# Kernel tuning notes

Measured on AMD Instinct MI355X. Metric: run time of the kernel, lower is better.

Reference implementation:

```python
import jax, jax.numpy as jnp
import numpy as np

N, D, H = 2048, 1024, 16
DH = D // H
LN_EPS = 1e-5


def setup_inputs() -> dict:
    key = jax.random.key(0)
    ks = jax.random.split(key, 12)
    s = 1.0 / np.sqrt(D)
    return {
        "ht": jax.random.normal(ks[0], (N, D), jnp.float32),
        "attention_mask": jnp.ones((1, N), jnp.float32),
        "Wq": jax.random.normal(ks[1], (D, D), jnp.float32) * s,
        "bq": jnp.zeros((D,), jnp.float32),
        "Wk": jax.random.normal(ks[2], (D, D), jnp.float32) * s,
        "bk": jnp.zeros((D,), jnp.float32),
        "Wv": jax.random.normal(ks[3], (D, D), jnp.float32) * s,
        "bv": jnp.zeros((D,), jnp.float32),
        "Wd": jax.random.normal(ks[4], (D, D), jnp.float32) * s,
        "bd": jnp.zeros((D,), jnp.float32),
        "gamma": jnp.ones((D,), jnp.float32),
        "beta": jnp.zeros((D,), jnp.float32),
    }


def reference(ht, attention_mask, Wq, bq, Wk, bk, Wv, bv, Wd, bd, gamma, beta):
    # ht: [N, D] -> batch of 1: [1, N, D]
    x = ht[None]
    # QKV projections, split into heads: [1, N, H, DH]
    q = (x @ Wq.T + bq).reshape(1, N, H, DH)
    k = (x @ Wk.T + bk).reshape(1, N, H, DH)
    v = (x @ Wv.T + bv).reshape(1, N, H, DH)
    # attention scores [1, H, N, N]
    scores = jnp.einsum("bnhd,bmhd->bhnm", q, k) / jnp.sqrt(jnp.asarray(DH, x.dtype))
    # 2D mask -> [B, 1, 1, N], additive form (1 - m) * -10000
    ext_mask = (1.0 - attention_mask)[:, None, None, :] * -10000.0
    scores = scores + ext_mask
    probs = jax.nn.softmax(scores, axis=-1)
    # context [1, N, H, DH] -> [N, D]
    ctx = jnp.einsum("bhnm,bmhd->bnhd", probs, v).reshape(1, N, D)[0]
    # dense + tanh (dropout p=0 is identity) + residual
    sht = jnp.tanh(ctx @ Wd.T + bd) + ht
    # LayerNorm over last dim
    mu = jnp.mean(sht, axis=-1, keepdims=True)
    var = jnp.var(sht, axis=-1, keepdims=True)
    return (sht - mu) / jnp.sqrt(var + LN_EPS) * gamma + beta
```

## Files before the change

kernel.cpp:

```cpp
#include <hip/hip_runtime.h>
#include <hip/hip_bf16.h>
#include <math.h>

#define N_TOK 2048
#define DMODEL 1024
#define NHEAD 16
#define DHEAD 64
#define LN_EPS 1e-5f
#define LOG2E 1.44269504f

typedef __attribute__((ext_vector_type(8))) short short8;
typedef __attribute__((ext_vector_type(4))) float f32x4;
typedef __attribute__((ext_vector_type(16))) float f32x16;

__device__ inline unsigned short f2bf(float f) {
    union { float f; unsigned u; } v; v.f = f;
    unsigned r = v.u + 0x7FFF + ((v.u >> 16) & 1);
    return (unsigned short)(r >> 16);
}

__device__ inline float bf2f(unsigned short b) {
    union { unsigned u; float f; } v; v.u = ((unsigned)b) << 16;
    return v.f;
}
// ... 74 lines not shown
    int srow = l >> 3;
    int ssc = (((l & 7) ^ srow) << 3);

    f32x4 acc[4][2] = {};

    for (int k0 = 0; k0 < DMODEL; k0 += 64) {
        #pragma unroll
        for (int c = 0; c < 2; ++c) {
            int ci = (w << 1) | c;
            int r = (ci << 3) | srow;
            gld16(X + (size_t)(row0 + r) * DMODEL + k0 + ssc, As + ci * 512);
        }
        #pragma unroll
        for (int c = 0; c < 4; ++c) {
            int ci = (w << 2) | c;
            int r = (ci << 3) | srow;
            gld16(W + (size_t)(wcol0 + r) * DMODEL + k0 + ssc, Bs + ci * 512);
        }
        __syncthreads();
        #pragma unroll
        for (int kk = 0; kk < 64; kk += 32) {
            short8 af[4], bf[2];
            #pragma unroll
            for (int m = 0; m < 4; ++m)
                af[m] = *reinterpret_cast<const short8*>(
                    As + (m * 16 + lr) * 64 + ((((kk >> 3) + lk) ^ (lr & 7)) << 3));
            #pragma unroll
            for (int n = 0; n < 2; ++n)
                bf[n] = *reinterpret_cast<const short8*>(
                    Bs + (wc + n * 16 + lr) * 64 + ((((kk >> 3) + lk) ^ (lr & 7)) << 3));
            #pragma unroll
            for (int m = 0; m < 4; ++m)
                #pragma unroll
                for (int n = 0; n < 2; ++n)
                    acc[m][n] = __builtin_amdgcn_mfma_f32_16x16x32_bf16(af[m], bf[n], acc[m][n], 0, 0, 0);
        }
        __syncthreads();
    }

    if (mat == 2) {
        #pragma unroll
        for (int n = 0; n < 2; ++n) {
            int dl = wc + n * 16 + lr;
            float bia = bias[wcol0 + dl];
            #pragma unroll
            for (int m = 0; m < 4; ++m) {
                #pragma unroll
                for (int r = 0; r < 4; ++r) {
                    int nl = m * 16 + lk * 4 + r;
                    Bs[dl * 72 + nl] = f2bf(acc[m][n][r] + bia);
                }
            }
        }
        __syncthreads();
        #pragma unroll
        for (int it = 0; it < 4; ++it) {
            int slot = it * 256 + t;
            int dl = slot >> 3, nb = slot & 7;
            short8 v = *reinterpret_cast<const short8*>(Bs + dl * 72 + nb * 8);
            *reinterpret_cast<short8*>(VT + (size_t)(wcol0 + dl) * N_TOK + row0 + nb * 8) = v;
        }
    } else {
        unsigned short* O = (mat == 0) ? Q : K;
        #pragma unroll
        for (int n = 0; n < 2; ++n) {
            int ccol = wcol0 + wc + n * 16 + lr;
            float bia = bias[ccol];
            #pragma unroll
            for (int m = 0; m < 4; ++m) {
                #pragma unroll
                for (int r = 0; r < 4; ++r) {
                    int rowg = row0 + m * 16 + lk * 4 + r;
                    O[(size_t)rowg * DMODEL + ccol] = f2bf((acc[m][n][r] + bia) * osc);
                }
            }
        }
    }
}

__global__ __launch_bounds__(256) void attn32(
    const unsigned short* __restrict__ Q, const unsigned short* __restrict__ K,
    const unsigned short* __restrict__ VT, const float* __restrict__ madd,
    unsigned short* __restrict__ P0, unsigned short* __restrict__ P1,
    float* __restrict__ Mm, float* __restrict__ Ml)
{
    __shared__ __align__(16) unsigned short Kt[2][2][4096];
    __shared__ __align__(16) unsigned short Vt[2][2][4096];
    __shared__ __align__(16) float Mt[2][128];

    int p = blockIdx.x;
    int work = (p & 7) * 64 + (p >> 3);
    int h = (work >> 4) & 15;
    int hb = h * DHEAD;
    int z = work >> 8;
    int kbase = z << 10;
    int t = threadIdx.x, w = t >> 6, l = t & 63;
    int lo5 = l & 31, hi = l >> 5;
    int qw = (work & 15) * 128 + w * 32;

    short8 qf[4];
    #pragma unroll
    for (int ds = 0; ds < 4; ++ds)
        qf[ds] = *reinterpret_cast<const short8*>(
            Q + (size_t)(qw + lo5) * DMODEL + hb + ds * 16 + hi * 8);

    short8 ones8;
    #pragma unroll
    for (int j = 0; j < 8; ++j) ones8[j] = (short)0x3F80;

    f32x16 ctx0 = {}, ctx1 = {}, ctxS = {};
    float mrow = -1e30f;

#define STAGE(kt_, buf_) do {                                                   \
        int k0s = kbase + (kt_) * 128;                                          \
        _Pragma("unroll")                                                       \
        for (int sub = 0; sub < 2; ++sub) {                                     \
            _Pragma("unroll")                                                   \
            for (int c = 0; c < 2; ++c) {                                       \
                int ci = (w << 1) | c;                                          \
                int rr = (ci << 3) | (l >> 3);                                  \
                int sc = (((l & 7) ^ (rr & 7)) << 3);                           \
                gld16(K + (size_t)(k0s + sub * 64 + rr) * DMODEL + hb + sc,     \
                      &Kt[buf_][sub][ci * 512]);                                \
                gld16(VT + (size_t)(hb + rr) * N_TOK + k0s + sub * 64 + sc,     \
                      &Vt[buf_][sub][ci * 512]);                                \
            }                                                                   \
        }                                                                       \
        if (t < 32) gld16((const unsigned short*)(madd + k0s + l * 4),          \
                          (unsigned short*)&Mt[buf_][0]);                       \
    } while (0)

    STAGE(0, 0);
    __syncthreads();

    int cb = 0;
    for (int kt = 0; kt < 8; ++kt) {
        if (kt + 1 < 8) STAGE(kt + 1, cb ^ 1);

        #pragma unroll
        for (int sub = 0; sub < 2; ++sub) {
            const unsigned short* Kc = &Kt[cb][sub][0];
            const unsigned short* Vc = &Vt[cb][sub][0];
            const float* Mc = &Mt[cb][sub * 64];

            f32x16 s0, s1;
            #pragma unroll
            for (int rg = 0; rg < 4; ++rg) {
                f32x4 a = *reinterpret_cast<const f32x4*>(Mc + 8 * rg + 4 * hi);
                f32x4 b = *reinterpret_cast<const f32x4*>(Mc + 32 + 8 * rg + 4 * hi);
                #pragma unroll
                for (int j = 0; j < 4; ++j) { s0[4 * rg + j] = a[j]; s1[4 * rg + j] = b[j]; }
            }

            __builtin_amdgcn_s_setprio(1);
            #pragma unroll
            for (int ds = 0; ds < 4; ++ds) {
                short8 a0 = *reinterpret_cast<const short8*>(
                    Kc + (size_t)lo5 * 64 + (((2 * ds + hi) ^ (l & 7)) << 3));
                s0 = __builtin_amdgcn_mfma_f32_32x32x16_bf16(a0, qf[ds], s0, 0, 0, 0);
            }
            #pragma unroll
            for (int ds = 0; ds < 4; ++ds) {
                short8 a1 = *reinterpret_cast<const short8*>(
                    Kc + (size_t)(32 + lo5) * 64 + (((2 * ds + hi) ^ (l & 7)) << 3));
                s1 = __builtin_amdgcn_mfma_f32_32x32x16_bf16(a1, qf[ds], s1, 0, 0, 0);
            }
            __builtin_amdgcn_s_setprio(0);

            float u0 = mx3(s0[0], s0[1], s0[2]);
            float u1 = mx3(s0[3], s0[4], s0[5]);
            float u2 = mx3(s0[6], s0[7], s0[8]);
            float u3 = mx3(s0[9], s0[10], s0[11]);
            float u4 = mx3(s0[12], s0[13], s0[14]);
            float u5 = mx3(s0[15], s1[0], s1[1]);
            float u6 = mx3(s1[2], s1[3], s1[4]);
            float u7 = mx3(s1[5], s1[6], s1[7]);
            float u8 = mx3(s1[8], s1[9], s1[10]);
            float u9 = mx3(s1[11], s1[12], s1[13]);
            float ua = fmaxf(s1[14], s1[15]);
            float v0_ = mx3(u0, u1, u2);
            float v1_ = mx3(u3, u4, u5);
            float v2_ = mx3(u6, u7, u8);
            float tm = mx3(v0_, v1_, mx3(v2_, u9, ua));
            tm = fmaxf(tm, __shfl_xor(tm, 32));

            if (__any(tm > mrow + 8.0f)) {
                float mnew = fmaxf(mrow, tm);
                float sc = __builtin_amdgcn_exp2f(mrow - mnew);
                mrow = mnew;
                #pragma unroll
                for (int reg = 0; reg < 16; ++reg) {
                    float scr = __shfl(sc, (reg & 3) + 8 * (reg >> 2) + 4 * hi);
                    ctx0[reg] *= scr; ctx1[reg] *= scr; ctxS[reg] *= scr;
                }
            }

            unsigned u[2][4][2];
            #pragma unroll
            for (int g = 0; g < 4; ++g) {
                float p0 = __builtin_amdgcn_exp2f(s0[4 * g + 0] - mrow);
                float p1 = __builtin_amdgcn_exp2f(s0[4 * g + 1] - mrow);
                float p2 = __builtin_amdgcn_exp2f(s0[4 * g + 2] - mrow);
                float p3 = __builtin_amdgcn_exp2f(s0[4 * g + 3] - mrow);
                u[0][g][0] = cvtpk_bf16(p0, p1);
                u[0][g][1] = cvtpk_bf16(p2, p3);
                float q0_ = __builtin_amdgcn_exp2f(s1[4 * g + 0] - mrow);
                float q1_ = __builtin_amdgcn_exp2f(s1[4 * g + 1] - mrow);
                float q2_ = __builtin_amdgcn_exp2f(s1[4 * g + 2] - mrow);
                float q3_ = __builtin_amdgcn_exp2f(s1[4 * g + 3] - mrow);
                u[1][g][0] = cvtpk_bf16(q0_, q1_);
                u[1][g][1] = cvtpk_bf16(q2_, q3_);
            }

            short8 pa[4];
            #pragma unroll
            for (int nb = 0; nb < 2; ++nb) {
                #pragma unroll
                for (int ks = 0; ks < 2; ++ks) {
                    auto r0 = __builtin_amdgcn_permlane32_swap(u[nb][2 * ks][0], u[nb][2 * ks + 1][0], false, false);
                    auto r1 = __builtin_amdgcn_permlane32_swap(u[nb][2 * ks][1], u[nb][2 * ks + 1][1], false, false);
                    union { unsigned uu[4]; short8 v; } pu;
                    pu.uu[0] = r0[0]; pu.uu[1] = r1[0]; pu.uu[2] = r0[1]; pu.uu[3] = r1[1];
                    pa[nb * 2 + ks] = pu.v;
                }
            }

            __builtin_amdgcn_s_setprio(1);
            #pragma unroll
            for (int ks = 0; ks < 4; ++ks) {
                short8 v0 = *reinterpret_cast<const short8*>(
                    Vc + (size_t)lo5 * 64 + (((2 * ks + hi) ^ (l & 7)) << 3));
                ctx0 = __builtin_amdgcn_mfma_f32_32x32x16_bf16(pa[ks], v0, ctx0, 0, 0, 0);
                short8 v1 = *reinterpret_cast<const short8*>(
                    Vc + (size_t)(32 + lo5) * 64 + (((2 * ks + hi) ^ (l & 7)) << 3));
                ctx1 = __builtin_amdgcn_mfma_f32_32x32x16_bf16(pa[ks], v1, ctx1, 0, 0, 0);
                ctxS = __builtin_amdgcn_mfma_f32_32x32x16_bf16(pa[ks], ones8, ctxS, 0, 0, 0);
            }
            __builtin_amdgcn_s_setprio(0);
        }

        __syncthreads();
        cb ^= 1;
    }
#undef STAGE

    unsigned short* P = z ? P1 : P0;
    #pragma unroll
    for (int reg = 0; reg < 16; ++reg) {
        float inv = 1.0f / ctxS[reg];
        int row = qw + (reg & 3) + 8 * (reg >> 2) + 4 * hi;
        P[(size_t)row * DMODEL + hb + lo5]      = f2bf(ctx0[reg] * inv);
        P[(size_t)row * DMODEL + hb + 32 + lo5] = f2bf(ctx1[reg] * inv);
    }
    int mlb = z * (NHEAD * N_TOK) + h * N_TOK + qw;
    if (l < 32) Mm[mlb + l] = mrow;
    #pragma unroll
    for (int reg = 0; reg < 16; ++reg) {
        int q = (reg & 3) + 8 * (reg >> 2) + 4 * hi;
        if (lo5 == reg) Ml[mlb + q] = ctxS[reg];
    }
}

__global__ __launch_bounds__(256) void attn_combine(
    const unsigned short* __restrict__ P0, const unsigned short* __restrict__ P1,
    const float* __restrict__ Mm, const float* __restrict__ Ml,
    unsigned short* __restrict__ Ctx)
{
    int tok = blockIdx.x;
    int t = threadIdx.x;
    int d = t * 4;
    int h = t >> 4;
    int i0 = h * N_TOK + tok;
    int i1 = NHEAD * N_TOK + i0;
    float m0 = Mm[i0], m1 = Mm[i1];
    float l0 = Ml[i0], l1 = Ml[i1];
    float m = fmaxf(m0, m1);
    float w0 = l0 * __builtin_amdgcn_exp2f(m0 - m);
    float w1 = l1 * __builtin_amdgcn_exp2f(m1 - m);
    float inv = 1.0f / (w0 + w1);
    w0 *= inv; w1 *= inv;
    ushort4 c0 = *reinterpret_cast<const ushort4*>(P0 + (size_t)tok * DMODEL + d);
    ushort4 c1 = *reinterpret_cast<const ushort4*>(P1 + (size_t)tok * DMODEL + d);
    ushort4 o;
    o.x = f2bf(bf2f(c0.x) * w0 + bf2f(c1.x) * w1);
    o.y = f2bf(bf2f(c0.y) * w0 + bf2f(c1.y) * w1);
    o.z = f2bf(bf2f(c0.z) * w0 + bf2f(c1.z) * w1);
    o.w = f2bf(bf2f(c0.w) * w0 + bf2f(c1.w) * w1);
    *reinterpret_cast<ushort4*>(Ctx + (size_t)tok * DMODEL + d) = o;
}

__global__ __launch_bounds__(256) void gemm_dense(
    const unsigned short* __restrict__ X, const unsigned short* __restrict__ W,
    const float* __restrict__ bias, const float* __restrict__ ht,
    float* __restrict__ Sht)
{
    __shared__ __align__(16) unsigned short As[64 * 64];
    __shared__ __align__(16) unsigned short Bs[64 * 64];
    int p = blockIdx.x;
    int work = (p & 7) * 64 + (p >> 3);
    int row0 = (work % 32) * 64;
    int col0 = (work / 32) * 64;

    int t = threadIdx.x, w = t >> 6, l = t & 63;
    int lr = l & 15, lk = l >> 4;
    int wc = w * 16;
    int srow = l >> 3;
    int ssc = (((l & 7) ^ srow) << 3);

    f32x4 acc[4] = {};

    for (int k0 = 0; k0 < DMODEL; k0 += 64) {
        #pragma unroll
        for (int c = 0; c < 2; ++c) {
            int ci = (w << 1) | c;
            int r = (ci << 3) | srow;
            gld16(X + (size_t)(row0 + r) * DMODEL + k0 + ssc, As + ci * 512);
            gld16(W + (size_t)(col0 + r) * DMODEL + k0 + ssc, Bs + ci * 512);
        }
        __syncthreads();
        #pragma unroll
        for (int kk = 0; kk < 64; kk += 32) {
            short8 af[4], bf0;
            #pragma unroll
            for (int m = 0; m < 4; ++m)
                af[m] = *reinterpret_cast<const short8*>(
                    As + (m * 16 + lr) * 64 + ((((kk >> 3) + lk) ^ (lr & 7)) << 3));
            bf0 = *reinterpret_cast<const short8*>(
                Bs + (wc + lr) * 64 + ((((kk >> 3) + lk) ^ (lr & 7)) << 3));
            #pragma unroll
            for (int m = 0; m < 4; ++m)
                acc[m] = __builtin_amdgcn_mfma_f32_16x16x32_bf16(af[m], bf0, acc[m], 0, 0, 0);
        }
        __syncthreads();
    }

    int col = col0 + wc + lr;
    float bia = bias[col];
    #pragma unroll
    for (int m = 0; m < 4; ++m) {
        #pragma unroll
        for (int r = 0; r < 4; ++r) {
            int rowg = row0 + m * 16 + lk * 4 + r;
            float x2 = 2.0f * (acc[m][r] + bia);
            float th = 1.0f - 2.0f / (1.0f + __expf(x2));
            Sht[(size_t)rowg * DMODEL + col] = th + ht[(size_t)rowg * DMODEL + col];
        }
    }
}

__global__ __launch_bounds__(256) void layernorm(
    const float* __restrict__ S, const float* __restrict__ gamma,
    const float* __restrict__ beta, float* __restrict__ out)
{
    int row = blockIdx.x;
    int t = threadIdx.x;
    const float* x = S + (size_t)row * DMODEL;
    float4 v = *reinterpret_cast<const float4*>(x + t * 4);
    float sum = v.x + v.y + v.z + v.w;
    float sq = v.x * v.x + v.y * v.y + v.z * v.z + v.w * v.w;
    #pragma unroll
    for (int d = 1; d < 64; d <<= 1) { sum += __shfl_xor(sum, d); sq += __shfl_xor(sq, d); }
    __shared__ float ssum[4], ssq[4];
    int w = t >> 6, l = t & 63;
    if (l == 0) { ssum[w] = sum; ssq[w] = sq; }
    __syncthreads();
    sum = ssum[0] + ssum[1] + ssum[2] + ssum[3];
    sq = ssq[0] + ssq[1] + ssq[2] + ssq[3];
    float mu = sum / DMODEL;
    float var = sq / DMODEL - mu * mu;
    float inv = rsqrtf(var + LN_EPS);
    float4 g = *reinterpret_cast<const float4*>(gamma + t * 4);
    float4 b = *reinterpret_cast<const float4*>(beta + t * 4);
    float4 o;
    o.x = (v.x - mu) * inv * g.x + b.x;
    o.y = (v.y - mu) * inv * g.y + b.y;
    o.z = (v.z - mu) * inv * g.z + b.z;
    o.w = (v.w - mu) * inv * g.w + b.w;
    *reinterpret_cast<float4*>(out + (size_t)row * DMODEL + t * 4) = o;
}

extern "C" void kernel_launch(void* const* d_in, const int* in_sizes, int n_in,
                              void* d_out, int out_size, void* d_ws, size_t ws_size,
                              hipStream_t stream) {
    const float* ht   = (const float*)d_in[0];
    const float* mask = (const float*)d_in[1];
    const float* Wq   = (const float*)d_in[2];
    const float* bq   = (const float*)d_in[3];
    const float* Wk   = (const float*)d_in[4];
    const float* bk   = (const float*)d_in[5];
    const float* Wv   = (const float*)d_in[6];
    const float* bv   = (const float*)d_in[7];
    const float* Wd   = (const float*)d_in[8];
    const float* bd   = (const float*)d_in[9];
    const float* gamma= (const float*)d_in[10];
    const float* beta = (const float*)d_in[11];
    float* out = (float*)d_out;

    char* ws = (char*)d_ws;
    const size_t MB = 1024 * 1024;
    unsigned short* Xb  = (unsigned short*)(ws + 0 * MB);
    unsigned short* Wqb = (unsigned short*)(ws + 4 * MB);
    unsigned short* Wkb = (unsigned short*)(ws + 6 * MB);
    unsigned short* Wvb = (unsigned short*)(ws + 8 * MB);
    unsigned short* Wdb = (unsigned short*)(ws + 10 * MB);
    unsigned short* Qb  = (unsigned short*)(ws + 12 * MB);
    unsigned short* Kb  = (unsigned short*)(ws + 16 * MB);
    unsigned short* Vb  = (unsigned short*)(ws + 20 * MB);
    unsigned short* VTb = (unsigned short*)(ws + 24 * MB);
    unsigned short* Ctxb= (unsigned short*)(ws + 28 * MB);
    float* maddb        = (float*)(ws + 32 * MB);
    unsigned short* Pctx0 = Xb;
    unsigned short* Pctx1 = Vb;
    float* Mm           = (float*)(ws + 4 * MB);
    float* Ml           = (float*)(ws + 4 * MB + 256 * 1024);
    float* Sht          = (float*)(ws + 12 * MB);

    cvt_all<<<6146, 256, 0, stream>>>(ht, Wq, Wk, Wv, Wd, mask,
                                      Xb, Wqb, Wkb, Wvb, Wdb, maddb);

    gemm_qkv<<<768, 256, 0, stream>>>(Xb, Wqb, Wkb, Wvb, bq, bk, bv, Qb, Kb, VTb);

    attn32<<<512, 256, 0, stream>>>(Qb, Kb, VTb, maddb, Pctx0, Pctx1, Mm, Ml);

    attn_combine<<<N_TOK, 256, 0, stream>>>(Pctx0, Pctx1, Mm, Ml, Ctxb);

    gemm_dense<<<512, 256, 0, stream>>>(Ctxb, Wdb, bd, ht, Sht);

    layernorm<<<N_TOK, 256, 0, stream>>>(Sht, gamma, beta, out);
}
```

Measured before the change: 84.25 us.

## Split attention KV range four ways instead of two for more blocks

Raises the flash-decoding style KV split from 2 to 4 chunks of 512 keys, doubling the attention grid to 1024 blocks, with each block handling 64-key tiles and preloading its whole mask slice once. The combine kernel now merges four partial contexts using per-split max and sum. The goal is better CU occupancy and latency hiding on the attention pass. In exchange it adds more partial-output traffic and combine work, shrinks the per-iteration tile, and reshuffles workspace aliasing (Wqb, VTb and others reused as scratch).

```diff
diff --git a/kernel.cpp b/kernel.cpp
--- a/kernel.cpp
+++ b/kernel.cpp
@@ -180,18 +180,19 @@
     const unsigned short* __restrict__ Q, const unsigned short* __restrict__ K,
     const unsigned short* __restrict__ VT, const float* __restrict__ madd,
     unsigned short* __restrict__ P0, unsigned short* __restrict__ P1,
+    unsigned short* __restrict__ P2, unsigned short* __restrict__ P3,
     float* __restrict__ Mm, float* __restrict__ Ml)
 {
-    __shared__ __align__(16) unsigned short Kt[2][2][4096];
-    __shared__ __align__(16) unsigned short Vt[2][2][4096];
-    __shared__ __align__(16) float Mt[2][128];
+    __shared__ __align__(16) unsigned short Kt[2][4096];
+    __shared__ __align__(16) unsigned short Vt[2][4096];
+    __shared__ __align__(16) float Mt[512];
 
     int p = blockIdx.x;
-    int work = (p & 7) * 64 + (p >> 3);
+    int work = (p & 7) * 128 + (p >> 3);
     int h = (work >> 4) & 15;
     int hb = h * DHEAD;
     int z = work >> 8;
-    int kbase = z << 10;
+    int kbase = z << 9;
     int t = threadIdx.x, w = t >> 6, l = t & 63;
     int lo5 = l & 31, hi = l >> 5;
     int qw = (work & 15) * 128 + w * 32;
@@ -209,23 +210,21 @@
     f32x16 ctx0 = {}, ctx1 = {}, ctxS = {};
     float mrow = -1e30f;
 
+    if (t < 128) {
+        gld16((const unsigned short*)(madd + kbase + t * 4),
+              (unsigned short*)&Mt[(t >> 6) * 256]);
+    }
+
 #define STAGE(kt_, buf_) do {                                                   \
-        int k0s = kbase + (kt_) * 128;                                          \
+        int k0s = kbase + (kt_) * 64;                                           \
         _Pragma("unroll")                                                       \
-        for (int sub = 0; sub < 2; ++sub) {                                     \
-            _Pragma("unroll")                                                   \
-            for (int c = 0; c < 2; ++c) {                                       \
-                int ci = (w << 1) | c;                                          \
-                int rr = (ci << 3) | (l >> 3);                                  \
-                int sc = (((l & 7) ^ (rr & 7)) << 3);                           \
-                gld16(K + (size_t)(k0s + sub * 64 + rr) * DMODEL + hb + sc,     \
-                      &Kt[buf_][sub][ci * 512]);                                \
-                gld16(VT + (size_t)(hb + rr) * N_TOK + k0s + sub * 64 + sc,     \
-                      &Vt[buf_][sub][ci * 512]);                                \
-            }                                                                   \
+        for (int c = 0; c < 2; ++c) {                                           \
+            int ci = (w << 1) | c;                                              \
+            int rr = (ci << 3) | (l >> 3);                                      \
+            int sc = (((l & 7) ^ (rr & 7)) << 3);                               \
+            gld16(K + (size_t)(k0s + rr) * DMODEL + hb + sc, &Kt[buf_][ci * 512]); \
+            gld16(VT + (size_t)(hb + rr) * N_TOK + k0s + sc, &Vt[buf_][ci * 512]); \
         }                                                                       \
-        if (t < 32) gld16((const unsigned short*)(madd + k0s + l * 4),          \
-                          (unsigned short*)&Mt[buf_][0]);                       \
     } while (0)
 
     STAGE(0, 0);
@@ -235,114 +234,111 @@
     for (int kt = 0; kt < 8; ++kt) {
         if (kt + 1 < 8) STAGE(kt + 1, cb ^ 1);
 
-        #pragma unroll
-        for (int sub = 0; sub < 2; ++sub) {
-            const unsigned short* Kc = &Kt[cb][sub][0];
-            const unsigned short* Vc = &Vt[cb][sub][0];
-            const float* Mc = &Mt[cb][sub * 64];
-
-            f32x16 s0, s1;
-            #pragma unroll
-            for (int rg = 0; rg < 4; ++rg) {
-                f32x4 a = *reinterpret_cast<const f32x4*>(Mc + 8 * rg + 4 * hi);
-                f32x4 b = *reinterpret_cast<const f32x4*>(Mc + 32 + 8 * rg + 4 * hi);
-                #pragma unroll
-                for (int j = 0; j < 4; ++j) { s0[4 * rg + j] = a[j]; s1[4 * rg + j] = b[j]; }
+        const unsigned short* Kc = &Kt[cb][0];
+        const unsigned short* Vc = &Vt[cb][0];
+        const float* Mc = &Mt[kt * 64];
+
+        f32x16 s0, s1;
+        #pragma unroll
+        for (int rg = 0; rg < 4; ++rg) {
+            f32x4 a = *reinterpret_cast<const f32x4*>(Mc + 8 * rg + 4 * hi);
+            f32x4 b = *reinterpret_cast<const f32x4*>(Mc + 32 + 8 * rg + 4 * hi);
+            #pragma unroll
+            for (int j = 0; j < 4; ++j) { s0[4 * rg + j] = a[j]; s1[4 * rg + j] = b[j]; }
+        }
+
+        __builtin_amdgcn_s_setprio(1);
+        #pragma unroll
+        for (int ds = 0; ds < 4; ++ds) {
+            short8 a0 = *reinterpret_cast<const short8*>(
+                Kc + (size_t)lo5 * 64 + (((2 * ds + hi) ^ (l & 7)) << 3));
+            s0 = __builtin_amdgcn_mfma_f32_32x32x16_bf16(a0, qf[ds], s0, 0, 0, 0);
+        }
+        #pragma unroll
+        for (int ds = 0; ds < 4; ++ds) {
+            short8 a1 = *reinterpret_cast<const short8*>(
+                Kc + (size_t)(32 + lo5) * 64 + (((2 * ds + hi) ^ (l & 7)) << 3));
+            s1 = __builtin_amdgcn_mfma_f32_32x32x16_bf16(a1, qf[ds], s1, 0, 0, 0);
+        }
+        __builtin_amdgcn_s_setprio(0);
+
+        float u0 = mx3(s0[0], s0[1], s0[2]);
+        float u1 = mx3(s0[3], s0[4], s0[5]);
+        float u2 = mx3(s0[6], s0[7], s0[8]);
+        float u3 = mx3(s0[9], s0[10], s0[11]);
+        float u4 = mx3(s0[12], s0[13], s0[14]);
+        float u5 = mx3(s0[15], s1[0], s1[1]);
+        float u6 = mx3(s1[2], s1[3], s1[4]);
+        float u7 = mx3(s1[5], s1[6], s1[7]);
+        float u8 = mx3(s1[8], s1[9], s1[10]);
+        float u9 = mx3(s1[11], s1[12], s1[13]);
+        float ua = fmaxf(s1[14], s1[15]);
+        float v0_ = mx3(u0, u1, u2);
+        float v1_ = mx3(u3, u4, u5);
+        float v2_ = mx3(u6, u7, u8);
+        float tm = mx3(v0_, v1_, mx3(v2_, u9, ua));
+        tm = fmaxf(tm, __shfl_xor(tm, 32));
+
+        if (__any(tm > mrow + 8.0f)) {
+            float mnew = fmaxf(mrow, tm);
+            float sc = __builtin_amdgcn_exp2f(mrow - mnew);
+            mrow = mnew;
+            #pragma unroll
+            for (int reg = 0; reg < 16; ++reg) {
+                float scr = __shfl(sc, (reg & 3) + 8 * (reg >> 2) + 4 * hi);
+                ctx0[reg] *= scr; ctx1[reg] *= scr; ctxS[reg] *= scr;
             }
-
-            __builtin_amdgcn_s_setprio(1);
-            #pragma unroll
-            for (int ds = 0; ds < 4; ++ds) {
-                short8 a0 = *reinterpret_cast<const short8*>(
-                    Kc + (size_t)lo5 * 64 + (((2 * ds + hi) ^ (l & 7)) << 3));
-                s0 = __builtin_amdgcn_mfma_f32_32x32x16_bf16(a0, qf[ds], s0, 0, 0, 0);
+        }
+
+        unsigned u[2][4][2];
+        #pragma unroll
+        for (int g = 0; g < 4; ++g) {
+            float p0 = __builtin_amdgcn_exp2f(s0[4 * g + 0] - mrow);
+            float p1 = __builtin_amdgcn_exp2f(s0[4 * g + 1] - mrow);
+            float p2 = __builtin_amdgcn_exp2f(s0[4 * g + 2] - mrow);
+            float p3 = __builtin_amdgcn_exp2f(s0[4 * g + 3] - mrow);
+            u[0][g][0] = cvtpk_bf16(p0, p1);
+            u[0][g][1] = cvtpk_bf16(p2, p3);
+            float q0_ = __builtin_amdgcn_exp2f(s1[4 * g + 0] - mrow);
+            float q1_ = __builtin_amdgcn_exp2f(s1[4 * g + 1] - mrow);
+            float q2_ = __builtin_amdgcn_exp2f(s1[4 * g + 2] - mrow);
+            float q3_ = __builtin_amdgcn_exp2f(s1[4 * g + 3] - mrow);
+            u[1][g][0] = cvtpk_bf16(q0_, q1_);
+            u[1][g][1] = cvtpk_bf16(q2_, q3_);
+        }
+
+        short8 pa[4];
+        #pragma unroll
+        for (int nb = 0; nb < 2; ++nb) {
+            #pragma unroll
+            for (int ks = 0; ks < 2; ++ks) {
+                auto r0 = __builtin_amdgcn_permlane32_swap(u[nb][2 * ks][0], u[nb][2 * ks + 1][0], false, false);
+                auto r1 = __builtin_amdgcn_permlane32_swap(u[nb][2 * ks][1], u[nb][2 * ks + 1][1], false, false);
+                union { unsigned uu[4]; short8 v; } pu;
+                pu.uu[0] = r0[0]; pu.uu[1] = r1[0]; pu.uu[2] = r0[1]; pu.uu[3] = r1[1];
+                pa[nb * 2 + ks] = pu.v;
             }
-            #pragma unroll
-            for (int ds = 0; ds < 4; ++ds) {
-                short8 a1 = *reinterpret_cast<const short8*>(
-                    Kc + (size_t)(32 + lo5) * 64 + (((2 * ds + hi) ^ (l & 7)) << 3));
-                s1 = __builtin_amdgcn_mfma_f32_32x32x16_bf16(a1, qf[ds], s1, 0, 0, 0);
-            }
-            __builtin_amdgcn_s_setprio(0);
-
-            float u0 = mx3(s0[0], s0[1], s0[2]);
-            float u1 = mx3(s0[3], s0[4], s0[5]);
-            float u2 = mx3(s0[6], s0[7], s0[8]);
-            float u3 = mx3(s0[9], s0[10], s0[11]);
-            float u4 = mx3(s0[12], s0[13], s0[14]);
-            float u5 = mx3(s0[15], s1[0], s1[1]);
-            float u6 = mx3(s1[2], s1[3], s1[4]);
-            float u7 = mx3(s1[5], s1[6], s1[7]);
-            float u8 = mx3(s1[8], s1[9], s1[10]);
-            float u9 = mx3(s1[11], s1[12], s1[13]);
-            float ua = fmaxf(s1[14], s1[15]);
-            float v0_ = mx3(u0, u1, u2);
-            float v1_ = mx3(u3, u4, u5);
-            float v2_ = mx3(u6, u7, u8);
-            float tm = mx3(v0_, v1_, mx3(v2_, u9, ua));
-            tm = fmaxf(tm, __shfl_xor(tm, 32));
-
-            if (__any(tm > mrow + 8.0f)) {
-                float mnew = fmaxf(mrow, tm);
-                float sc = __builtin_amdgcn_exp2f(mrow - mnew);
-                mrow = mnew;
-                #pragma unroll
-                for (int reg = 0; reg < 16; ++reg) {
-                    float scr = __shfl(sc, (reg & 3) + 8 * (reg >> 2) + 4 * hi);
-                    ctx0[reg] *= scr; ctx1[reg] *= scr; ctxS[reg] *= scr;
-                }
-            }
-
-            unsigned u[2][4][2];
-            #pragma unroll
-            for (int g = 0; g < 4; ++g) {
-                float p0 = __builtin_amdgcn_exp2f(s0[4 * g + 0] - mrow);
-                float p1 = __builtin_amdgcn_exp2f(s0[4 * g + 1] - mrow);
-                float p2 = __builtin_amdgcn_exp2f(s0[4 * g + 2] - mrow);
-                float p3 = __builtin_amdgcn_exp2f(s0[4 * g + 3] - mrow);
-                u[0][g][0] = cvtpk_bf16(p0, p1);
-                u[0][g][1] = cvtpk_bf16(p2, p3);
-                float q0_ = __builtin_amdgcn_exp2f(s1[4 * g + 0] - mrow);
-                float q1_ = __builtin_amdgcn_exp2f(s1[4 * g + 1] - mrow);
-                float q2_ = __builtin_amdgcn_exp2f(s1[4 * g + 2] - mrow);
-                float q3_ = __builtin_amdgcn_exp2f(s1[4 * g + 3] - mrow);
-                u[1][g][0] = cvtpk_bf16(q0_, q1_);
-                u[1][g][1] = cvtpk_bf16(q2_, q3_);
-            }
-
-            short8 pa[4];
-            #pragma unroll
-            for (int nb = 0; nb < 2; ++nb) {
-                #pragma unroll
-                for (int ks = 0; ks < 2; ++ks) {
-                    auto r0 = __builtin_amdgcn_permlane32_swap(u[nb][2 * ks][0], u[nb][2 * ks + 1][0], false, false);
-                    auto r1 = __builtin_amdgcn_permlane32_swap(u[nb][2 * ks][1], u[nb][2 * ks + 1][1], false, false);
-                    union { unsigned uu[4]; short8 v; } pu;
-                    pu.uu[0] = r0[0]; pu.uu[1] = r1[0]; pu.uu[2] = r0[1]; pu.uu[3] = r1[1];
-                    pa[nb * 2 + ks] = pu.v;
-                }
-            }
-
-            __builtin_amdgcn_s_setprio(1);
-            #pragma unroll
-            for (int ks = 0; ks < 4; ++ks) {
-                short8 v0 = *reinterpret_cast<const short8*>(
-                    Vc + (size_t)lo5 * 64 + (((2 * ks + hi) ^ (l & 7)) << 3));
-                ctx0 = __builtin_amdgcn_mfma_f32_32x32x16_bf16(pa[ks], v0, ctx0, 0, 0, 0);
-                short8 v1 = *reinterpret_cast<const short8*>(
-                    Vc + (size_t)(32 + lo5) * 64 + (((2 * ks + hi) ^ (l & 7)) << 3));
-                ctx1 = __builtin_amdgcn_mfma_f32_32x32x16_bf16(pa[ks], v1, ctx1, 0, 0, 0);
-                ctxS = __builtin_amdgcn_mfma_f32_32x32x16_bf16(pa[ks], ones8, ctxS, 0, 0, 0);
-            }
-            __builtin_amdgcn_s_setprio(0);
-        }
+        }
+
+        __builtin_amdgcn_s_setprio(1);
+        #pragma unroll
+        for (int ks = 0; ks < 4; ++ks) {
+            short8 v0 = *reinterpret_cast<const short8*>(
+                Vc + (size_t)lo5 * 64 + (((2 * ks + hi) ^ (l & 7)) << 3));
+            ctx0 = __builtin_amdgcn_mfma_f32_32x32x16_bf16(pa[ks], v0, ctx0, 0, 0, 0);
+            short8 v1 = *reinterpret_cast<const short8*>(
+                Vc + (size_t)(32 + lo5) * 64 + (((2 * ks + hi) ^ (l & 7)) << 3));
+            ctx1 = __builtin_amdgcn_mfma_f32_32x32x16_bf16(pa[ks], v1, ctx1, 0, 0, 0);
+            ctxS = __builtin_amdgcn_mfma_f32_32x32x16_bf16(pa[ks], ones8, ctxS, 0, 0, 0);
+        }
+        __builtin_amdgcn_s_setprio(0);
 
         __syncthreads();
         cb ^= 1;
     }
 #undef STAGE
 
-    unsigned short* P = z ? P1 : P0;
+    unsigned short* P = (z == 0) ? P0 : (z == 1) ? P1 : (z == 2) ? P2 : P3;
     #pragma unroll
     for (int reg = 0; reg < 16; ++reg) {
         float inv = 1.0f / ctxS[reg];
@@ -361,6 +357,7 @@
 
 __global__ __launch_bounds__(256) void attn_combine(
     const unsigned short* __restrict__ P0, const unsigned short* __restrict__ P1,
+    const unsigned short* __restrict__ P2, const unsigned short* __restrict__ P3,
     const float* __restrict__ Mm, const float* __restrict__ Ml,
     unsigned short* __restrict__ Ctx)
 {
@@ -369,21 +366,25 @@
     int d = t * 4;
     int h = t >> 4;
     int i0 = h * N_TOK + tok;
-    int i1 = NHEAD * N_TOK + i0;
-    float m0 = Mm[i0], m1 = Mm[i1];
-    float l0 = Ml[i0], l1 = Ml[i1];
-    float m = fmaxf(m0, m1);
+    const int S = NHEAD * N_TOK;
+    float m0 = Mm[i0], m1 = Mm[i0 + S], m2 = Mm[i0 + 2 * S], m3 = Mm[i0 + 3 * S];
+    float l0 = Ml[i0], l1 = Ml[i0 + S], l2 = Ml[i0 + 2 * S], l3 = Ml[i0 + 3 * S];
+    float m = fmaxf(fmaxf(m0, m1), fmaxf(m2, m3));
     float w0 = l0 * __builtin_amdgcn_exp2f(m0 - m);
     float w1 = l1 * __builtin_amdgcn_exp2f(m1 - m);
-    float inv = 1.0f / (w0 + w1);
-    w0 *= inv; w1 *= inv;
+    float w2 = l2 * __builtin_amdgcn_exp2f(m2 - m);
+    float w3 = l3 * __builtin_amdgcn_exp2f(m3 - m);
+    float inv = 1.0f / (w0 + w1 + w2 + w3);
+    w0 *= inv; w1 *= inv; w2 *= inv; w3 *= inv;
     ushort4 c0 = *reinterpret_cast<const ushort4*>(P0 + (size_t)tok * DMODEL + d);
     ushort4 c1 = *reinterpret_cast<const ushort4*>(P1 + (size_t)tok * DMODEL + d);
+    ushort4 c2 = *reinterpret_cast<const ushort4*>(P2 + (size_t)tok * DMODEL + d);
+    ushort4 c3 = *reinterpret_cast<const ushort4*>(P3 + (size_t)tok * DMODEL + d);
     ushort4 o;
-    o.x = f2bf(bf2f(c0.x) * w0 + bf2f(c1.x) * w1);
-    o.y = f2bf(bf2f(c0.y) * w0 + bf2f(c1.y) * w1);
-    o.z = f2bf(bf2f(c0.z) * w0 + bf2f(c1.z) * w1);
-    o.w = f2bf(bf2f(c0.w) * w0 + bf2f(c1.w) * w1);
+    o.x = f2bf(bf2f(c0.x) * w0 + bf2f(c1.x) * w1 + bf2f(c2.x) * w2 + bf2f(c3.x) * w3);
+    o.y = f2bf(bf2f(c0.y) * w0 + bf2f(c1.y) * w1 + bf2f(c2.y) * w2 + bf2f(c3.y) * w3);
+    o.z = f2bf(bf2f(c0.z) * w0 + bf2f(c1.z) * w1 + bf2f(c2.z) * w2 + bf2f(c3.z) * w3);
+    o.w = f2bf(bf2f(c0.w) * w0 + bf2f(c1.w) * w1 + bf2f(c2.w) * w2 + bf2f(c3.w) * w3);
     *reinterpret_cast<ushort4*>(Ctx + (size_t)tok * DMODEL + d) = o;
 }
 
@@ -505,12 +506,14 @@
     unsigned short* Kb  = (unsigned short*)(ws + 16 * MB);
     unsigned short* Vb  = (unsigned short*)(ws + 20 * MB);
     unsigned short* VTb = (unsigned short*)(ws + 24 * MB);
-    unsigned short* Ctxb= (unsigned short*)(ws + 28 * MB);
     float* maddb        = (float*)(ws + 32 * MB);
     unsigned short* Pctx0 = Xb;
     unsigned short* Pctx1 = Vb;
-    float* Mm           = (float*)(ws + 4 * MB);
-    float* Ml           = (float*)(ws + 4 * MB + 256 * 1024);
+    unsigned short* Pctx2 = Wqb;
+    unsigned short* Pctx3 = (unsigned short*)(ws + 28 * MB);
+    float* Mm           = (float*)(ws + 8 * MB);
+    float* Ml           = (float*)(ws + 8 * MB + 512 * 1024);
+    unsigned short* Ctxb= VTb;
     float* Sht          = (float*)(ws + 12 * MB);
 
     cvt_all<<<6146, 256, 0, stream>>>(ht, Wq, Wk, Wv, Wd, mask,
@@ -518,9 +521,10 @@
 
     gemm_qkv<<<768, 256, 0, stream>>>(Xb, Wqb, Wkb, Wvb, bq, bk, bv, Qb, Kb, VTb);
 
-    attn32<<<512, 256, 0, stream>>>(Qb, Kb, VTb, maddb, Pctx0, Pctx1, Mm, Ml);
-
-    attn_combine<<<N_TOK, 256, 0, stream>>>(Pctx0, Pctx1, Mm, Ml, Ctxb);
+    attn32<<<1024, 256, 0, stream>>>(Qb, Kb, VTb, maddb,
+                                     Pctx0, Pctx1, Pctx2, Pctx3, Mm, Ml);
+
+    attn_combine<<<N_TOK, 256, 0, stream>>>(Pctx0, Pctx1, Pctx2, Pctx3, Mm, Ml, Ctxb);
 
     gemm_dense<<<512, 256, 0, stream>>>(Ctxb, Wdb, bd, ht, Sht);
 
```

Result: slower. 90.13 us (+7.0%).

## Triple-buffer K/V tiles with 64-key stages and explicit vmcnt waits in attention

Applied to the files above, without the earlier changes.

Restructures the attention kernel's K/V staging from double-buffered 128-key tiles to a three-slot ring of 64-key tiles, prefetching two stages ahead. The full 1024-entry mask slice is loaded once up front instead of per stage. __syncthreads is replaced with raw s_barrier plus s_waitcnt vmcnt counts, so a new load can be issued while earlier ones are still outstanding. This aims to hide global-load latency better at similar LDS use, but it adds more barriers per key and depends on the hand-counted vmcnt values being correct.

```diff
diff --git a/kernel.cpp b/kernel.cpp
--- a/kernel.cpp
+++ b/kernel.cpp
@@ -182,9 +182,9 @@
     unsigned short* __restrict__ P0, unsigned short* __restrict__ P1,
     float* __restrict__ Mm, float* __restrict__ Ml)
 {
-    __shared__ __align__(16) unsigned short Kt[2][2][4096];
-    __shared__ __align__(16) unsigned short Vt[2][2][4096];
-    __shared__ __align__(16) float Mt[2][128];
+    __shared__ __align__(16) unsigned short Kt[3][4096];
+    __shared__ __align__(16) unsigned short Vt[3][4096];
+    __shared__ __align__(16) float Mt[1024];
 
     int p = blockIdx.x;
     int work = (p & 7) * 64 + (p >> 3);
@@ -210,135 +210,140 @@
     float mrow = -1e30f;
 
 #define STAGE(kt_, buf_) do {                                                   \
-        int k0s = kbase + (kt_) * 128;                                          \
+        int k0s = kbase + (kt_) * 64;                                           \
         _Pragma("unroll")                                                       \
-        for (int sub = 0; sub < 2; ++sub) {                                     \
-            _Pragma("unroll")                                                   \
-            for (int c = 0; c < 2; ++c) {                                       \
-                int ci = (w << 1) | c;                                          \
-                int rr = (ci << 3) | (l >> 3);                                  \
-                int sc = (((l & 7) ^ (rr & 7)) << 3);                           \
-                gld16(K + (size_t)(k0s + sub * 64 + rr) * DMODEL + hb + sc,     \
-                      &Kt[buf_][sub][ci * 512]);                                \
-                gld16(VT + (size_t)(hb + rr) * N_TOK + k0s + sub * 64 + sc,     \
-                      &Vt[buf_][sub][ci * 512]);                                \
-            }                                                                   \
+        for (int c = 0; c < 2; ++c) {                                           \
+            int ci = (w << 1) | c;                                              \
+            int rr = (ci << 3) | (l >> 3);                                      \
+            int sc = (((l & 7) ^ (rr & 7)) << 3);                               \
+            gld16(K + (size_t)(k0s + rr) * DMODEL + hb + sc, &Kt[buf_][ci * 512]); \
+            gld16(VT + (size_t)(hb + rr) * N_TOK + k0s + sc, &Vt[buf_][ci * 512]); \
         }                                                                       \
-        if (t < 32) gld16((const unsigned short*)(madd + k0s + l * 4),          \
-                          (unsigned short*)&Mt[buf_][0]);                       \
     } while (0)
 
+    gld16((const unsigned short*)(madd + kbase + t * 4), (unsigned short*)&Mt[w * 256]);
     STAGE(0, 0);
-    __syncthreads();
+    STAGE(1, 1);
+    __builtin_amdgcn_sched_barrier(0);
+    asm volatile("s_waitcnt vmcnt(4)");
+    __builtin_amdgcn_s_barrier();
+    __builtin_amdgcn_sched_barrier(0);
 
     int cb = 0;
-    for (int kt = 0; kt < 8; ++kt) {
-        if (kt + 1 < 8) STAGE(kt + 1, cb ^ 1);
-
-        #pragma unroll
-        for (int sub = 0; sub < 2; ++sub) {
-            const unsigned short* Kc = &Kt[cb][sub][0];
-            const unsigned short* Vc = &Vt[cb][sub][0];
-            const float* Mc = &Mt[cb][sub * 64];
-
-            f32x16 s0, s1;
-            #pragma unroll
-            for (int rg = 0; rg < 4; ++rg) {
-                f32x4 a = *reinterpret_cast<const f32x4*>(Mc + 8 * rg + 4 * hi);
-                f32x4 b = *reinterpret_cast<const f32x4*>(Mc + 32 + 8 * rg + 4 * hi);
-                #pragma unroll
-                for (int j = 0; j < 4; ++j) { s0[4 * rg + j] = a[j]; s1[4 * rg + j] = b[j]; }
+    for (int kt = 0; kt < 16; ++kt) {
+        const unsigned short* Kc = &Kt[cb][0];
+        const unsigned short* Vc = &Vt[cb][0];
+        const float* Mc = &Mt[kt * 64];
+
+        f32x16 s0, s1;
+        #pragma unroll
+        for (int rg = 0; rg < 4; ++rg) {
+            f32x4 a = *reinterpret_cast<const f32x4*>(Mc + 8 * rg + 4 * hi);
+            f32x4 b = *reinterpret_cast<const f32x4*>(Mc + 32 + 8 * rg + 4 * hi);
+            #pragma unroll
+            for (int j = 0; j < 4; ++j) { s0[4 * rg + j] = a[j]; s1[4 * rg + j] = b[j]; }
+        }
+
+        __builtin_amdgcn_s_setprio(1);
+        #pragma unroll
+        for (int ds = 0; ds < 4; ++ds) {
+            short8 a0 = *reinterpret_cast<const short8*>(
+                Kc + (size_t)lo5 * 64 + (((2 * ds + hi) ^ (l & 7)) << 3));
+            s0 = __builtin_amdgcn_mfma_f32_32x32x16_bf16(a0, qf[ds], s0, 0, 0, 0);
+        }
+        #pragma unroll
+        for (int ds = 0; ds < 4; ++ds) {
+            short8 a1 = *reinterpret_cast<const short8*>(
+                Kc + (size_t)(32 + lo5) * 64 + (((2 * ds + hi) ^ (l & 7)) << 3));
+            s1 = __builtin_amdgcn_mfma_f32_32x32x16_bf16(a1, qf[ds], s1, 0, 0, 0);
+        }
+        __builtin_amdgcn_s_setprio(0);
+
+        float u0 = mx3(s0[0], s0[1], s0[2]);
+        float u1 = mx3(s0[3], s0[4], s0[5]);
+        float u2 = mx3(s0[6], s0[7], s0[8]);
+        float u3 = mx3(s0[9], s0[10], s0[11]);
+        float u4 = mx3(s0[12], s0[13], s0[14]);
+        float u5 = mx3(s0[15], s1[0], s1[1]);
+        float u6 = mx3(s1[2], s1[3], s1[4]);
+        float u7 = mx3(s1[5], s1[6], s1[7]);
+        float u8 = mx3(s1[8], s1[9], s1[10]);
+        float u9 = mx3(s1[11], s1[12], s1[13]);
+        float ua = fmaxf(s1[14], s1[15]);
+        float v0_ = mx3(u0, u1, u2);
+        float v1_ = mx3(u3, u4, u5);
+        float v2_ = mx3(u6, u7, u8);
+        float tm = mx3(v0_, v1_, mx3(v2_, u9, ua));
+        tm = fmaxf(tm, __shfl_xor(tm, 32));
+
+        if (__any(tm > mrow + 8.0f)) {
+            float mnew = fmaxf(mrow, tm);
+            float sc = __builtin_amdgcn_exp2f(mrow - mnew);
+            mrow = mnew;
+            #pragma unroll
+            for (int reg = 0; reg < 16; ++reg) {
+                float scr = __shfl(sc, (reg & 3) + 8 * (reg >> 2) + 4 * hi);
+                ctx0[reg] *= scr; ctx1[reg] *= scr; ctxS[reg] *= scr;
             }
-
-            __builtin_amdgcn_s_setprio(1);
-            #pragma unroll
-            for (int ds = 0; ds < 4; ++ds) {
-                short8 a0 = *reinterpret_cast<const short8*>(
-                    Kc + (size_t)lo5 * 64 + (((2 * ds + hi) ^ (l & 7)) << 3));
-                s0 = __builtin_amdgcn_mfma_f32_32x32x16_bf16(a0, qf[ds], s0, 0, 0, 0);
+        }
+
+        unsigned u[2][4][2];
+        #pragma unroll
+        for (int g = 0; g < 4; ++g) {
+            float p0 = __builtin_amdgcn_exp2f(s0[4 * g + 0] - mrow);
+            float p1 = __builtin_amdgcn_exp2f(s0[4 * g + 1] - mrow);
+            float p2 = __builtin_amdgcn_exp2f(s0[4 * g + 2] - mrow);
+            float p3 = __builtin_amdgcn_exp2f(s0[4 * g + 3] - mrow);
+            u[0][g][0] = cvtpk_bf16(p0, p1);
+            u[0][g][1] = cvtpk_bf16(p2, p3);
+            float q0_ = __builtin_amdgcn_exp2f(s1[4 * g + 0] - mrow);
+            float q1_ = __builtin_amdgcn_exp2f(s1[4 * g + 1] - mrow);
+            float q2_ = __builtin_amdgcn_exp2f(s1[4 * g + 2] - mrow);
+            float q3_ = __builtin_amdgcn_exp2f(s1[4 * g + 3] - mrow);
+            u[1][g][0] = cvtpk_bf16(q0_, q1_);
+            u[1][g][1] = cvtpk_bf16(q2_, q3_);
+        }
+
+        short8 pa[4];
+        #pragma unroll
+        for (int nb = 0; nb < 2; ++nb) {
+            #pragma unroll
+            for (int ks = 0; ks < 2; ++ks) {
+                auto r0 = __builtin_amdgcn_permlane32_swap(u[nb][2 * ks][0], u[nb][2 * ks + 1][0], false, false);
+                auto r1 = __builtin_amdgcn_permlane32_swap(u[nb][2 * ks][1], u[nb][2 * ks + 1][1], false, false);
+                union { unsigned uu[4]; short8 v; } pu;
+                pu.uu[0] = r0[0]; pu.uu[1] = r1[0]; pu.uu[2] = r0[1]; pu.uu[3] = r1[1];
+                pa[nb * 2 + ks] = pu.v;
             }
-            #pragma unroll
-            for (int ds = 0; ds < 4; ++ds) {
-                short8 a1 = *reinterpret_cast<const short8*>(
-                    Kc + (size_t)(32 + lo5) * 64 + (((2 * ds + hi) ^ (l & 7)) << 3));
-                s1 = __builtin_amdgcn_mfma_f32_32x32x16_bf16(a1, qf[ds], s1, 0, 0, 0);
-            }
-            __builtin_amdgcn_s_setprio(0);
-
-            float u0 = mx3(s0[0], s0[1], s0[2]);
-            float u1 = mx3(s0[3], s0[4], s0[5]);
-            float u2 = mx3(s0[6], s0[7], s0[8]);
-            float u3 = mx3(s0[9], s0[10], s0[11]);
-            float u4 = mx3(s0[12], s0[13], s0[14]);
-            float u5 = mx3(s0[15], s1[0], s1[1]);
-            float u6 = mx3(s1[2], s1[3], s1[4]);
-            float u7 = mx3(s1[5], s1[6], s1[7]);
-            float u8 = mx3(s1[8], s1[9], s1[10]);
-            float u9 = mx3(s1[11], s1[12], s1[13]);
-            float ua = fmaxf(s1[14], s1[15]);
-            float v0_ = mx3(u0, u1, u2);
-            float v1_ = mx3(u3, u4, u5);
-            float v2_ = mx3(u6, u7, u8);
-            float tm = mx3(v0_, v1_, mx3(v2_, u9, ua));
-            tm = fmaxf(tm, __shfl_xor(tm, 32));
-
-            if (__any(tm > mrow + 8.0f)) {
-                float mnew = fmaxf(mrow, tm);
-                float sc = __builtin_amdgcn_exp2f(mrow - mnew);
-                mrow = mnew;
-                #pragma unroll
-                for (int reg = 0; reg < 16; ++reg) {
-                    float scr = __shfl(sc, (reg & 3) + 8 * (reg >> 2) + 4 * hi);
-                    ctx0[reg] *= scr; ctx1[reg] *= scr; ctxS[reg] *= scr;
-                }
-            }
-
-            unsigned u[2][4][2];
-            #pragma unroll
-            for (int g = 0; g < 4; ++g) {
-                float p0 = __builtin_amdgcn_exp2f(s0[4 * g + 0] - mrow);
-                float p1 = __builtin_amdgcn_exp2f(s0[4 * g + 1] - mrow);
-                float p2 = __builtin_amdgcn_exp2f(s0[4 * g + 2] - mrow);
-                float p3 = __builtin_amdgcn_exp2f(s0[4 * g + 3] - mrow);
-                u[0][g][0] = cvtpk_bf16(p0, p1);
-                u[0][g][1] = cvtpk_bf16(p2, p3);
-                float q0_ = __builtin_amdgcn_exp2f(s1[4 * g + 0] - mrow);
-                float q1_ = __builtin_amdgcn_exp2f(s1[4 * g + 1] - mrow);
-                float q2_ = __builtin_amdgcn_exp2f(s1[4 * g + 2] - mrow);
-                float q3_ = __builtin_amdgcn_exp2f(s1[4 * g + 3] - mrow);
-                u[1][g][0] = cvtpk_bf16(q0_, q1_);
-                u[1][g][1] = cvtpk_bf16(q2_, q3_);
-            }
-
-            short8 pa[4];
-            #pragma unroll
-            for (int nb = 0; nb < 2; ++nb) {
-                #pragma unroll
-                for (int ks = 0; ks < 2; ++ks) {
-                    auto r0 = __builtin_amdgcn_permlane32_swap(u[nb][2 * ks][0], u[nb][2 * ks + 1][0], false, false);
-                    auto r1 = __builtin_amdgcn_permlane32_swap(u[nb][2 * ks][1], u[nb][2 * ks + 1][1], false, false);
-                    union { unsigned uu[4]; short8 v; } pu;
-                    pu.uu[0] = r0[0]; pu.uu[1] = r1[0]; pu.uu[2] = r0[1]; pu.uu[3] = r1[1];
-                    pa[nb * 2 + ks] = pu.v;
-                }
-            }
-
-            __builtin_amdgcn_s_setprio(1);
-            #pragma unroll
-            for (int ks = 0; ks < 4; ++ks) {
-                short8 v0 = *reinterpret_cast<const short8*>(
-                    Vc + (size_t)lo5 * 64 + (((2 * ks + hi) ^ (l & 7)) << 3));
-                ctx0 = __builtin_amdgcn_mfma_f32_32x32x16_bf16(pa[ks], v0, ctx0, 0, 0, 0);
-                short8 v1 = *reinterpret_cast<const short8*>(
-                    Vc + (size_t)(32 + lo5) * 64 + (((2 * ks + hi) ^ (l & 7)) << 3));
-                ctx1 = __builtin_amdgcn_mfma_f32_32x32x16_bf16(pa[ks], v1, ctx1, 0, 0, 0);
-                ctxS = __builtin_amdgcn_mfma_f32_32x32x16_bf16(pa[ks], ones8, ctxS, 0, 0, 0);
-            }
-            __builtin_amdgcn_s_setprio(0);
-        }
-
-        __syncthreads();
-        cb ^= 1;
+        }
+
+        __builtin_amdgcn_s_setprio(1);
+        #pragma unroll
+        for (int ks = 0; ks < 4; ++ks) {
+            short8 v0 = *reinterpret_cast<const short8*>(
+                Vc + (size_t)lo5 * 64 + (((2 * ks + hi) ^ (l & 7)) << 3));
+            ctx0 = __builtin_amdgcn_mfma_f32_32x32x16_bf16(pa[ks], v0, ctx0, 0, 0, 0);
+            short8 v1 = *reinterpret_cast<const short8*>(
+                Vc + (size_t)(32 + lo5) * 64 + (((2 * ks + hi) ^ (l & 7)) << 3));
+            ctx1 = __builtin_amdgcn_mfma_f32_32x32x16_bf16(pa[ks], v1, ctx1, 0, 0, 0);
+            ctxS = __builtin_amdgcn_mfma_f32_32x32x16_bf16(pa[ks], ones8, ctxS, 0, 0, 0);
+        }
+        __builtin_amdgcn_s_setprio(0);
+
+        __builtin_amdgcn_s_barrier();
+        __builtin_amdgcn_sched_barrier(0);
+        if (kt + 2 < 16) {
+            int sb = cb + 2; if (sb >= 3) sb -= 3;
+            STAGE(kt + 2, sb);
+        }
+        if (kt + 1 < 16) {
+            __builtin_amdgcn_sched_barrier(0);
+            if (kt + 2 < 16) asm volatile("s_waitcnt vmcnt(4)");
+            else             asm volatile("s_waitcnt vmcnt(0)");
+            __builtin_amdgcn_s_barrier();
+            __builtin_amdgcn_sched_barrier(0);
+        }
+        cb = (cb == 2) ? 0 : cb + 1;
     }
 #undef STAGE
 
```

Result: no change. 84.40 us (+0.2%).

## Fuse split-KV attention combine into dense GEMM A-tile staging with double buffering

Applied to the files above, without the earlier changes.

Removes the separate attn_combine kernel. The dense GEMM now loads both partial context tiles and their softmax max/sum statistics, merges them in registers, and writes the combined bf16 A tile into shared memory. The main loop is restructured with double-buffered LDS, so the next tile's loads overlap the current MFMA work. This saves one launch and one full round trip of the context tensor through memory. In exchange, each GEMM block now redoes the combine for every column tile and reads the partials more times, and it uses more registers and LDS.

```diff
diff --git a/kernel.cpp b/kernel.cpp
--- a/kernel.cpp
+++ b/kernel.cpp
@@ -359,41 +359,14 @@
     }
 }
 
-__global__ __launch_bounds__(256) void attn_combine(
+__global__ __launch_bounds__(256) void gemm_dense(
     const unsigned short* __restrict__ P0, const unsigned short* __restrict__ P1,
     const float* __restrict__ Mm, const float* __restrict__ Ml,
-    unsigned short* __restrict__ Ctx)
+    const unsigned short* __restrict__ W, const float* __restrict__ bias,
+    const float* __restrict__ ht, float* __restrict__ Sht)
 {
-    int tok = blockIdx.x;
-    int t = threadIdx.x;
-    int d = t * 4;
-    int h = t >> 4;
-    int i0 = h * N_TOK + tok;
-    int i1 = NHEAD * N_TOK + i0;
-    float m0 = Mm[i0], m1 = Mm[i1];
-    float l0 = Ml[i0], l1 = Ml[i1];
-    float m = fmaxf(m0, m1);
-    float w0 = l0 * __builtin_amdgcn_exp2f(m0 - m);
-    float w1 = l1 * __builtin_amdgcn_exp2f(m1 - m);
-    float inv = 1.0f / (w0 + w1);
-    w0 *= inv; w1 *= inv;
-    ushort4 c0 = *reinterpret_cast<const ushort4*>(P0 + (size_t)tok * DMODEL + d);
-    ushort4 c1 = *reinterpret_cast<const ushort4*>(P1 + (size_t)tok * DMODEL + d);
-    ushort4 o;
-    o.x = f2bf(bf2f(c0.x) * w0 + bf2f(c1.x) * w1);
-    o.y = f2bf(bf2f(c0.y) * w0 + bf2f(c1.y) * w1);
-    o.z = f2bf(bf2f(c0.z) * w0 + bf2f(c1.z) * w1);
-    o.w = f2bf(bf2f(c0.w) * w0 + bf2f(c1.w) * w1);
-    *reinterpret_cast<ushort4*>(Ctx + (size_t)tok * DMODEL + d) = o;
-}
-
-__global__ __launch_bounds__(256) void gemm_dense(
-    const unsigned short* __restrict__ X, const unsigned short* __restrict__ W,
-    const float* __restrict__ bias, const float* __restrict__ ht,
-    float* __restrict__ Sht)
-{
-    __shared__ __align__(16) unsigned short As[64 * 64];
-    __shared__ __align__(16) unsigned short Bs[64 * 64];
+    __shared__ __align__(16) unsigned short As[2][64 * 64];
+    __shared__ __align__(16) unsigned short Bs[2][64 * 64];
     int p = blockIdx.x;
     int work = (p & 7) * 64 + (p >> 3);
     int row0 = (work % 32) * 64;
@@ -405,32 +378,89 @@
     int srow = l >> 3;
     int ssc = (((l & 7) ^ srow) << 3);
 
+    int r_[2], c8_[2];
+    #pragma unroll
+    for (int it = 0; it < 2; ++it) { int slot = it * 256 + t; r_[it] = slot >> 3; c8_[it] = slot & 7; }
+
     f32x4 acc[4] = {};
 
-    for (int k0 = 0; k0 < DMODEL; k0 += 64) {
-        #pragma unroll
-        for (int c = 0; c < 2; ++c) {
-            int ci = (w << 1) | c;
-            int r = (ci << 3) | srow;
-            gld16(X + (size_t)(row0 + r) * DMODEL + k0 + ssc, As + ci * 512);
-            gld16(W + (size_t)(col0 + r) * DMODEL + k0 + ssc, Bs + ci * 512);
-        }
-        __syncthreads();
+    short8 a0[2], a1[2];
+    float pm0[2], pm1[2], pl0[2], pl1[2];
+
+#define LOADA(k0_) do {                                                          \
+        _Pragma("unroll")                                                        \
+        for (int it = 0; it < 2; ++it) {                                         \
+            int tok = row0 + r_[it];                                             \
+            int i0 = ((k0_) >> 6) * N_TOK + tok;                                 \
+            int i1 = NHEAD * N_TOK + i0;                                         \
+            a0[it] = *reinterpret_cast<const short8*>(P0 + (size_t)tok * DMODEL + (k0_) + c8_[it] * 8); \
+            a1[it] = *reinterpret_cast<const short8*>(P1 + (size_t)tok * DMODEL + (k0_) + c8_[it] * 8); \
+            pm0[it] = Mm[i0]; pm1[it] = Mm[i1];                                  \
+            pl0[it] = Ml[i0]; pl1[it] = Ml[i1];                                  \
+        }                                                                        \
+    } while (0)
+
+#define WRITEA(buf_) do {                                                        \
+        _Pragma("unroll")                                                        \
+        for (int it = 0; it < 2; ++it) {                                         \
+            float mm = fmaxf(pm0[it], pm1[it]);                                  \
+            float w0_ = pl0[it] * __builtin_amdgcn_exp2f(pm0[it] - mm);          \
+            float w1_ = pl1[it] * __builtin_amdgcn_exp2f(pm1[it] - mm);          \
+            float inv_ = 1.0f / (w0_ + w1_);                                     \
+            w0_ *= inv_; w1_ *= inv_;                                            \
+            union { unsigned uu[4]; short8 v; } pu;                              \
+            _Pragma("unroll")                                                    \
+            for (int j = 0; j < 4; ++j) {                                        \
+                float e0 = bf2f((unsigned short)a0[it][2 * j]) * w0_             \
+                         + bf2f((unsigned short)a1[it][2 * j]) * w1_;            \
+                float e1 = bf2f((unsigned short)a0[it][2 * j + 1]) * w0_         \
+                         + bf2f((unsigned short)a1[it][2 * j + 1]) * w1_;        \
+                pu.uu[j] = cvtpk_bf16(e0, e1);                                   \
+            }                                                                    \
+            *reinterpret_cast<short8*>(                                          \
+                &As[buf_][r_[it] * 64 + ((c8_[it] ^ (r_[it] & 7)) << 3)]) = pu.v;\
+        }                                                                        \
+    } while (0)
+
+#define STAGEB(k0_, buf_) do {                                                   \
+        _Pragma("unroll")                                                        \
+        for (int c = 0; c < 2; ++c) {                                            \
+            int ci = (w << 1) | c;                                               \
+            int rr = (ci << 3) | srow;                                           \
+            gld16(W + (size_t)(col0 + rr) * DMODEL + (k0_) + ssc, &Bs[buf_][ci * 512]); \
+        }                                                                        \
+    } while (0)
+
+    LOADA(0);
+    STAGEB(0, 0);
+    WRITEA(0);
+    __syncthreads();
+
+    for (int k0i = 0; k0i < 16; ++k0i) {
+        int buf = k0i & 1;
+        bool more = (k0i + 1) < 16;
+        if (more) { LOADA((k0i + 1) * 64); STAGEB((k0i + 1) * 64, buf ^ 1); }
+
         #pragma unroll
         for (int kk = 0; kk < 64; kk += 32) {
             short8 af[4], bf0;
             #pragma unroll
             for (int m = 0; m < 4; ++m)
                 af[m] = *reinterpret_cast<const short8*>(
-                    As + (m * 16 + lr) * 64 + ((((kk >> 3) + lk) ^ (lr & 7)) << 3));
+                    &As[buf][(m * 16 + lr) * 64 + ((((kk >> 3) + lk) ^ (lr & 7)) << 3)]);
             bf0 = *reinterpret_cast<const short8*>(
-                Bs + (wc + lr) * 64 + ((((kk >> 3) + lk) ^ (lr & 7)) << 3));
+                &Bs[buf][(wc + lr) * 64 + ((((kk >> 3) + lk) ^ (lr & 7)) << 3)]);
             #pragma unroll
             for (int m = 0; m < 4; ++m)
                 acc[m] = __builtin_amdgcn_mfma_f32_16x16x32_bf16(af[m], bf0, acc[m], 0, 0, 0);
         }
+
+        if (more) WRITEA(buf ^ 1);
         __syncthreads();
     }
+#undef LOADA
+#undef WRITEA
+#undef STAGEB
 
     int col = col0 + wc + lr;
     float bia = bias[col];
@@ -505,7 +535,6 @@
     unsigned short* Kb  = (unsigned short*)(ws + 16 * MB);
     unsigned short* Vb  = (unsigned short*)(ws + 20 * MB);
     unsigned short* VTb = (unsigned short*)(ws + 24 * MB);
-    unsigned short* Ctxb= (unsigned short*)(ws + 28 * MB);
     float* maddb        = (float*)(ws + 32 * MB);
     unsigned short* Pctx0 = Xb;
     unsigned short* Pctx1 = Vb;
@@ -520,9 +549,7 @@
 
     attn32<<<512, 256, 0, stream>>>(Qb, Kb, VTb, maddb, Pctx0, Pctx1, Mm, Ml);
 
-    attn_combine<<<N_TOK, 256, 0, stream>>>(Pctx0, Pctx1, Mm, Ml, Ctxb);
-
-    gemm_dense<<<512, 256, 0, stream>>>(Ctxb, Wdb, bd, ht, Sht);
+    gemm_dense<<<512, 256, 0, stream>>>(Pctx0, Pctx1, Mm, Ml, Wdb, bd, ht, Sht);
 
     layernorm<<<N_TOK, 256, 0, stream>>>(Sht, gamma, beta, out);
 }
```

Measured after the change: 88.96 us. 1.06x slower.
